# Kernel tuning notes

Measured on AMD Instinct MI355X. Metric: run time of the kernel, lower is better.

The kernel has to match this reference:

```python
import jax, jax.numpy as jnp
import numpy as np

H = W = 128  # render resolution (init height/width)
EPS = 1e-8

def _normalize(x, axis):
    return x / (jnp.linalg.norm(x, axis=axis, keepdims=True) + EPS)

def _render_one(pts, camrot, campos, proj, uv, faces):
    # pts (p,3), camrot (3,3), campos (3,), proj (3,1), uv (p,2), faces (f,3)
    pc = (pts - campos) @ camrot.T                       # camera-space verts (p,3)
    xy = pc[:, :2] * proj[:2, 0] / (pc[:, 2:3] + EPS)    # perspective projection -> NDC (p,2)
    v3d = pc[faces]                                      # (f,3,3)
    v2d = xy[faces]                                      # (f,3,2)
    n = jnp.cross(v3d[:, 1] - v3d[:, 0], v3d[:, 2] - v3d[:, 0])  # face normals (f,3)
    n1 = _normalize(n, axis=1)
    # pixel grid in NDC
    px = jnp.linspace(-1.0, 1.0, W)[None, None, :]
    py = jnp.linspace(1.0, -1.0, H)[None, :, None]
    ax, ay = v2d[:, 0, 0, None, None], v2d[:, 0, 1, None, None]
    bx, by = v2d[:, 1, 0, None, None], v2d[:, 1, 1, None, None]
    cx, cy = v2d[:, 2, 0, None, None], v2d[:, 2, 1, None, None]
    d = (by - cy) * (ax - cx) + (cx - bx) * (ay - cy)    # (f,1,1) signed 2*area
    l0 = ((by - cy) * (px - cx) + (cx - bx) * (py - cy)) / (d + EPS)
    l1 = ((cy - ay) * (px - cx) + (ax - cx) * (py - cy)) / (d + EPS)
    l2 = 1.0 - l0 - l1                                   # barycentrics (f,H,W)
    z = (l0 * v3d[:, 0, 2, None, None] + l1 * v3d[:, 1, 2, None, None]
         + l2 * v3d[:, 2, 2, None, None])                # interpolated depth (f,H,W)
    inside = (l0 >= 0) & (l1 >= 0) & (l2 >= 0) & (jnp.abs(d) > EPS) & (z > EPS)
    zm = jnp.where(inside, z, jnp.float32(1e10))
    idx = jnp.argmin(zm, axis=0)                         # nearest visible face per pixel (H,W)
    hard = jnp.any(inside, axis=0)[..., None].astype(pts.dtype)  # hardmask (H,W,1)
    take = lambda a: jnp.take_along_axis(a, idx[None], axis=0)[0]  # (H,W)
    uvsel = uv[faces][idx]                               # (H,W,3,2) per-pixel face uvs
    tc = (take(l0)[..., None] * uvsel[..., 0, :]
          + take(l1)[..., None] * uvsel[..., 1, :]
          + take(l2)[..., None] * uvsel[..., 2, :]) * hard  # imtexcoords (H,W,2)
    return tc, hard, n1

def _fragment_shader(tc, texture, mask):
    # nearest-filter texture lookup; texture (3,th,tw)
    th, tw = texture.shape[1], texture.shape[2]
    u = jnp.clip(tc[..., 0], 0.0, 1.0)
    v = jnp.clip(tc[..., 1], 0.0, 1.0)
    tx = jnp.round(u * (tw - 1)).astype(jnp.int32)
    ty = jnp.round((1.0 - v) * (th - 1)).astype(jnp.int32)
    color = texture[:, ty, tx].transpose(1, 2, 0)        # (H,W,3)
    return color * mask

def setup_inputs() -> dict:
    key = jax.random.key(0)
    ks = jax.random.split(key, 6)
    b, p, f = 3, 768, 1024
    points = jax.random.normal(ks[0], (b, p, 3), jnp.float32) * 0.3
    faces = jax.random.randint(ks[1], (f, 3), 0, p)
    camera_rot = jnp.broadcast_to(jnp.eye(3, dtype=jnp.float32), (b, 3, 3))
    camera_pos = jnp.zeros((b, 3), jnp.float32).at[:, 2].set(-3.0)  # objects in front of camera
    camera_proj = jnp.ones((3, 1), jnp.float32)
    uv = jax.random.uniform(ks[2], (b, p, 2), jnp.float32)
    texture = jax.random.uniform(ks[3], (b, 3, 512, 512), jnp.float32)
    ts = jax.random.normal(ks[4], (b, 3), jnp.float32)
    return dict(points=points, camera_rot=camera_rot, camera_pos=camera_pos,
                camera_proj=camera_proj, uv=uv, texture=texture, ts=ts, faces=faces)

def reference(points, camera_rot, camera_pos, camera_proj, uv, texture, ts, faces):
    b = points.shape[0]
    render = jax.vmap(_render_one, in_axes=(0, 0, 0, None, 0, None))
    tcs, masks, normals = render(points, camera_rot, camera_pos, camera_proj, uv, faces)
    ims = jax.vmap(_fragment_shader)(tcs, texture, masks)   # (b,H,W,3)
    probs = masks                                            # improb proxy == hardmask
    order = jnp.argsort(-ts[:, 2])                           # far -> near compositing order
    ims_s, probs_s, masks_s = ims[order], probs[order], masks[order]
    imrender, improb, fg = ims_s[0], probs_s[0], masks_s[0]
    for i in range(1, b):                                    # fixed small layer count
        m = masks_s[i] > 0.5
        imrender = jnp.where(m, ims_s[i], imrender)
        improb = jnp.where(m, probs_s[i], improb)
        fg = jnp.where(m, masks_s[i], fg)
    return imrender[None], improb[None], normals, fg[None]
```

## Files before the change

### kernel.cpp

```cpp
#include <hip/hip_runtime.h>
#include <math.h>

#define B_ 3
#define P_ 768
#define F_ 1024
#define H_ 128
#define W_ 128
#define HW_ (H_*W_)
#define EPS_ 1e-8f

#define OFF_PROB   49152
#define OFF_NORM   65536
#define OFF_FG     74752


__global__ __launch_bounds__(256) void raster_fwd(
    const float* __restrict__ points,
    const float* __restrict__ camrot,
    const float* __restrict__ campos,
    const float* __restrict__ proj,
    const int*   __restrict__ faces,
    float4* __restrict__ faceE,
    const float* __restrict__ uv,
    unsigned long long* __restrict__ packed,
    float*  __restrict__ normals_out)
{
#pragma clang fp contract(off)
    int wid  = blockIdx.x * 4 + (threadIdx.x >> 6);
    int sub  = blockIdx.y;
    int lane = threadIdx.x & 63;
    int b = wid / F_;
    int f = wid - b * F_;

    const float* R = camrot + b * 9;
    float cpx = campos[b*3+0], cpy = campos[b*3+1], cpz = campos[b*3+2];
    float pj0 = proj[0], pj1 = proj[1];

    int idx3[3];
    float pcx[3], pcy[3], pcz[3], sx[3], sy[3];
    for (int v = 0; v < 3; ++v) {
        int vi = faces[f*3 + v];
        idx3[v] = vi;
        const float* P = points + (b*P_ + vi) * 3;
        float vx = P[0] - cpx;
        float vy = P[1] - cpy;
        float vz = P[2] - cpz;
        float qx = (vx*R[0] + vy*R[1]) + vz*R[2];
        float qy = (vx*R[3] + vy*R[4]) + vz*R[5];
        float qz = (vx*R[6] + vy*R[7]) + vz*R[8];
        pcx[v] = qx; pcy[v] = qy; pcz[v] = qz;
        float dz = qz + EPS_;
        sx[v] = (qx * pj0) / dz;
        sy[v] = (qy * pj1) / dz;
    }

    float ax = sx[0], ay = sy[0];
    float bx = sx[1], by = sy[1];
    float cx = sx[2], cy = sy[2];

    float e0x = by - cy;
    float e0y = cx - bx;
    float e1x = cy - ay;
    float e1y = ax - cx;
    float d = e0x*(ax - cx) + e0y*(ay - cy);
    float denom = d + EPS_;
    bool valid = fabsf(d) > EPS_;
    float z0 = pcz[0], z1 = pcz[1], z2 = pcz[2];

    if (lane == 0 && sub == 0) {
        float4* rec = faceE + wid * 4;
        rec[0] = make_float4(e0x, e0y, e1x, e1y);
        rec[1] = make_float4(cx, cy, denom, valid ? 1.0f : 0.0f);
        const float* uvb = uv + b * P_ * 2;
        rec[2] = make_float4(uvb[idx3[0]*2+0], uvb[idx3[0]*2+1],
                             uvb[idx3[1]*2+0], uvb[idx3[1]*2+1]);
        rec[3] = make_float4(uvb[idx3[2]*2+0], uvb[idx3[2]*2+1], 0.0f, 0.0f);

        float ux = pcx[1]-pcx[0], uy = pcy[1]-pcy[0], uz = pcz[1]-pcz[0];
        float wx = pcx[2]-pcx[0], wy = pcy[2]-pcy[0], wz = pcz[2]-pcz[0];
        float nx = fmaf(uy, wz, -(uz*wy));
        float ny = fmaf(uz, wx, -(ux*wz));
        float nz = fmaf(ux, wy, -(uy*wx));
        float nn = sqrtf((nx*nx + ny*ny) + nz*nz) + 1e-8f;
        normals_out[wid*3+0] = nx / nn;
        normals_out[wid*3+1] = ny / nn;
        normals_out[wid*3+2] = nz / nn;
    }

    if (!valid) return;

    float gx0 = (ax + 1.0f) * 63.5f;
    float gx1 = (bx + 1.0f) * 63.5f;
    float gx2 = (cx + 1.0f) * 63.5f;
    float gy0 = (1.0f - ay) * 63.5f;
    float gy1 = (1.0f - by) * 63.5f;
    float gy2 = (1.0f - cy) * 63.5f;
    int xlo = max(0,   (int)ceilf (fminf(fminf(gx0,gx1),gx2) - 1.0f));
    int xhi = min(127, (int)floorf(fmaxf(fmaxf(gx0,gx1),gx2) + 1.0f));
    int ylo = max(0,   (int)ceilf (fminf(fminf(gy0,gy1),gy2) - 1.0f));
    int yhi = min(127, (int)floorf(fmaxf(fmaxf(gy0,gy1),gy2) + 1.0f));
    int wX = xhi - xlo + 1;
    int wY = yhi - ylo + 1;
    if (wX <= 0 || wY <= 0) return;
    int N = wX * wY;

    int i0 = sub * 64 + lane;
    if (i0 >= N) return;
    int q = 128 / wX;
    int r = 128 - q * wX;
    int yy = i0 / wX;
    int xx = i0 - yy * wX;

    const double STEP = 2.0 / 127.0;
    unsigned long long* cells = packed + b * HW_;

    for (int i = i0; i < N; i += 128) {
        int X = xlo + xx;
        int Y = ylo + yy;
        float px = (float)(-1.0 + (double)X * STEP);
        float py = (float)( 1.0 - (double)Y * STEP);
        float dx = px - cx;
        float dy = py - cy;
        float n0 = e0x*dx + e0y*dy;
        float n1 = e1x*dx + e1y*dy;
        float l0 = n0 / denom;
        float l1 = n1 / denom;
        float l2 = 1.0f - l0 - l1;
        float zz = (l0*z0 + l1*z1) + l2*z2;
        if (l0 >= 0.0f && l1 >= 0.0f && l2 >= 0.0f && zz > EPS_) {
            unsigned long long pk =
                ((unsigned long long)__float_as_uint(zz) << 32) | (unsigned)f;
            atomicMin(&cells[Y * W_ + X], pk);
        }
        xx += r; yy += q;
        if (xx >= wX) { xx -= wX; yy += 1; }
    }
}

__global__ __launch_bounds__(64) void shade_composite(
    const float4* __restrict__ faceE,
    const float*  __restrict__ tex,
    const float*  __restrict__ ts,
    const unsigned long long* __restrict__ packed,
    float* __restrict__ out)
{
#pragma clang fp contract(off)
    int pix = blockIdx.x * 64 + threadIdx.x;
    int y = pix >> 7;
    int x = pix & (W_ - 1);

    const double STEP = 2.0 / 127.0;
    float px = (float)(-1.0 + (double)x * STEP);
    float py = (float)( 1.0 - (double)y * STEP);

    const unsigned MISS_BITS = __float_as_uint(1e10f);

    unsigned long long pka = packed[0 * HW_ + pix];
    unsigned long long pkb = packed[1 * HW_ + pix];
    unsigned long long pkc = packed[2 * HW_ + pix];

    float k0 = ts[0*3+2], k1 = ts[1*3+2], k2 = ts[2*3+2];
    int o0 = 0, o1 = 1, o2 = 2;
    if (k1 > k0) { int ti=o0; o0=o1; o1=ti; float tf=k0; k0=k1; k1=tf; }
    if (k2 > k1) { int ti=o1; o1=o2; o2=ti; float tf=k1; k1=k2; k2=tf; }
    if (k1 > k0) { int ti=o0; o0=o1; o1=ti; float tf=k0; k0=k1; k1=tf; }

    unsigned long long p0 = (o0 == 0) ? pka : ((o0 == 1) ? pkb : pkc);
    unsigned long long p1 = (o1 == 0) ? pka : ((o1 == 1) ? pkb : pkc);
    unsigned long long p2 = (o2 == 0) ? pka : ((o2 == 1) ? pkb : pkc);
    bool h1 = (unsigned)(p1 >> 32) < MISS_BITS;
    bool h2 = (unsigned)(p2 >> 32) < MISS_BITS;

    int w = o0; unsigned long long pkw = p0;
    if (h1) { w = o1; pkw = p1; }
    if (h2) { w = o2; pkw = p2; }
    bool hardw = (unsigned)(pkw >> 32) < MISS_BITS;

    float sr = 0.0f, sg = 0.0f, sb = 0.0f, sm = 0.0f;
    if (hardw) {
        int fi = (int)(unsigned)pkw;
        const float4* rec = faceE + (w * F_ + fi) * 4;
        float4 A  = rec[0];
        float4 Bv = rec[1];
        float4 Cv = rec[2];
        float4 Dv = rec[3];

        float dx = px - Bv.x;
        float dy = py - Bv.y;
        float n0 = A.x*dx + A.y*dy;
        float n1 = A.z*dx + A.w*dy;
        float l0 = n0 / Bv.z;
        float l1 = n1 / Bv.z;
        float l2 = 1.0f - l0 - l1;
        float tu = (l0*Cv.x + l1*Cv.z) + l2*Dv.x;
        float tv = (l0*Cv.y + l1*Cv.w) + l2*Dv.y;
        float uc = fminf(fmaxf(tu, 0.0f), 1.0f);
        float vc = fminf(fmaxf(tv, 0.0f), 1.0f);
        int txi = (int)rintf(uc * 511.0f);
        int tyi = (int)rintf((1.0f - vc) * 511.0f);

        const float* tb = tex + w * 3 * 262144;
        int o = tyi*512 + txi;
        sr = tb[0*262144 + o];
        sg = tb[1*262144 + o];
        sb = tb[2*262144 + o];
        sm = 1.0f;
    }

    out[pix*3+0] = sr;
    out[pix*3+1] = sg;
    out[pix*3+2] = sb;
    out[OFF_PROB + pix] = sm;
    out[OFF_FG   + pix] = sm;
}

extern "C" void kernel_launch(void* const* d_in, const int* in_sizes, int n_in,
                              void* d_out, int out_size, void* d_ws, size_t ws_size,
                              hipStream_t stream) {
    const float* points = (const float*)d_in[0];
    const float* camrot = (const float*)d_in[1];
    const float* campos = (const float*)d_in[2];
    const float* proj   = (const float*)d_in[3];
    const float* uv     = (const float*)d_in[4];
    const float* tex    = (const float*)d_in[5];
    const float* ts     = (const float*)d_in[6];
    const int*   faces  = (const int*)d_in[7];
    float* out = (float*)d_out;

    char* ws = (char*)d_ws;
    float4* faceE = (float4*)(ws);
    unsigned long long* packed = (unsigned long long*)(ws + 196608);


    raster_fwd<<<dim3(B_*F_/4, 2), dim3(256), 0, stream>>>(
        points, camrot, campos, proj, faces, faceE, uv,
        packed, out + OFF_NORM);
    shade_composite<<<dim3(HW_/64), dim3(64), 0, stream>>>(
        faceE, tex, ts, packed, out);
}
```

Baseline: 83.83 us.

## Set up faces once per block and rasterize 16 faces with whole-block pixel loops

Raster work is remapped so each 256-thread block handles 16 faces. The first 16 threads compute the projection, edge equations, bounding box, face record and normal once per face and stage them in shared memory. After a block barrier, all 256 threads sweep each face's bounding box in turn. This removes the redundant per-lane setup (previously every lane of 2x64 threads recomputed each face) and the split grid. In exchange the grid shrinks to 192 blocks, faces inside a block are processed one after another, and small faces leave most threads idle.

```diff
diff --git a/kernel.cpp b/kernel.cpp
--- a/kernel.cpp
+++ b/kernel.cpp
@@ -8,6 +8,7 @@
 #define W_ 128
 #define HW_ (H_*W_)
 #define EPS_ 1e-8f
+#define FPB_ 16
 
 #define OFF_PROB   49152
 #define OFF_NORM   65536
@@ -26,48 +27,52 @@
     float*  __restrict__ normals_out)
 {
 #pragma clang fp contract(off)
-    int wid  = blockIdx.x * 4 + (threadIdx.x >> 6);
-    int sub  = blockIdx.y;
-    int lane = threadIdx.x & 63;
-    int b = wid / F_;
-    int f = wid - b * F_;
-
-    const float* R = camrot + b * 9;
-    float cpx = campos[b*3+0], cpy = campos[b*3+1], cpz = campos[b*3+2];
-    float pj0 = proj[0], pj1 = proj[1];
-
-    int idx3[3];
-    float pcx[3], pcy[3], pcz[3], sx[3], sy[3];
-    for (int v = 0; v < 3; ++v) {
-        int vi = faces[f*3 + v];
-        idx3[v] = vi;
-        const float* P = points + (b*P_ + vi) * 3;
-        float vx = P[0] - cpx;
-        float vy = P[1] - cpy;
-        float vz = P[2] - cpz;
-        float qx = (vx*R[0] + vy*R[1]) + vz*R[2];
-        float qy = (vx*R[3] + vy*R[4]) + vz*R[5];
-        float qz = (vx*R[6] + vy*R[7]) + vz*R[8];
-        pcx[v] = qx; pcy[v] = qy; pcz[v] = qz;
-        float dz = qz + EPS_;
-        sx[v] = (qx * pj0) / dz;
-        sy[v] = (qy * pj1) / dz;
-    }
-
-    float ax = sx[0], ay = sy[0];
-    float bx = sx[1], by = sy[1];
-    float cx = sx[2], cy = sy[2];
-
-    float e0x = by - cy;
-    float e0y = cx - bx;
-    float e1x = cy - ay;
-    float e1y = ax - cx;
-    float d = e0x*(ax - cx) + e0y*(ay - cy);
-    float denom = d + EPS_;
-    bool valid = fabsf(d) > EPS_;
-    float z0 = pcz[0], z1 = pcz[1], z2 = pcz[2];
-
-    if (lane == 0 && sub == 0) {
+    int tid = threadIdx.x;
+    int b   = blockIdx.x >> 6;
+
+    __shared__ float sE0x[FPB_], sE0y[FPB_], sE1x[FPB_], sE1y[FPB_];
+    __shared__ float sCx[FPB_],  sCy[FPB_],  sDen[FPB_];
+    __shared__ float sZ0[FPB_],  sZ1[FPB_],  sZ2[FPB_];
+    __shared__ int   sXlo[FPB_], sYlo[FPB_], sWX[FPB_], sN[FPB_];
+
+    if (tid < FPB_) {
+        int wid = blockIdx.x * FPB_ + tid;
+        int f   = wid - b * F_;
+
+        const float* R = camrot + b * 9;
+        float cpx = campos[b*3+0], cpy = campos[b*3+1], cpz = campos[b*3+2];
+        float pj0 = proj[0], pj1 = proj[1];
+
+        int idx3[3];
+        float pcx[3], pcy[3], pcz[3], sx[3], sy[3];
+        for (int v = 0; v < 3; ++v) {
+            int vi = faces[f*3 + v];
+            idx3[v] = vi;
+            const float* P = points + (b*P_ + vi) * 3;
+            float vx = P[0] - cpx;
+            float vy = P[1] - cpy;
+            float vz = P[2] - cpz;
+            float qx = (vx*R[0] + vy*R[1]) + vz*R[2];
+            float qy = (vx*R[3] + vy*R[4]) + vz*R[5];
+            float qz = (vx*R[6] + vy*R[7]) + vz*R[8];
+            pcx[v] = qx; pcy[v] = qy; pcz[v] = qz;
+            float dz = qz + EPS_;
+            sx[v] = (qx * pj0) / dz;
+            sy[v] = (qy * pj1) / dz;
+        }
+
+        float ax = sx[0], ay = sy[0];
+        float bx = sx[1], by = sy[1];
+        float cx = sx[2], cy = sy[2];
+
+        float e0x = by - cy;
+        float e0y = cx - bx;
+        float e1x = cy - ay;
+        float e1y = ax - cx;
+        float d = e0x*(ax - cx) + e0y*(ay - cy);
+        float denom = d + EPS_;
+        bool valid = fabsf(d) > EPS_;
+
         float4* rec = faceE + wid * 4;
         rec[0] = make_float4(e0x, e0y, e1x, e1y);
         rec[1] = make_float4(cx, cy, denom, valid ? 1.0f : 0.0f);
@@ -85,55 +90,71 @@
         normals_out[wid*3+0] = nx / nn;
         normals_out[wid*3+1] = ny / nn;
         normals_out[wid*3+2] = nz / nn;
+
+        int N = 0, xlo = 0, ylo = 0, wX = 1;
+        if (valid) {
+            float gx0 = (ax + 1.0f) * 63.5f;
+            float gx1 = (bx + 1.0f) * 63.5f;
+            float gx2 = (cx + 1.0f) * 63.5f;
+            float gy0 = (1.0f - ay) * 63.5f;
+            float gy1 = (1.0f - by) * 63.5f;
+            float gy2 = (1.0f - cy) * 63.5f;
+            xlo = max(0,   (int)ceilf (fminf(fminf(gx0,gx1),gx2) - 1.0f));
+            int xhi = min(127, (int)floorf(fmaxf(fmaxf(gx0,gx1),gx2) + 1.0f));
+            ylo = max(0,   (int)ceilf (fminf(fminf(gy0,gy1),gy2) - 1.0f));
+            int yhi = min(127, (int)floorf(fmaxf(fmaxf(gy0,gy1),gy2) + 1.0f));
+            int wXl = xhi - xlo + 1;
+            int wYl = yhi - ylo + 1;
+            if (wXl > 0 && wYl > 0) { N = wXl * wYl; wX = wXl; }
+        }
+        sE0x[tid] = e0x; sE0y[tid] = e0y; sE1x[tid] = e1x; sE1y[tid] = e1y;
+        sCx[tid]  = cx;  sCy[tid]  = cy;  sDen[tid] = denom;
+        sZ0[tid]  = pcz[0]; sZ1[tid] = pcz[1]; sZ2[tid] = pcz[2];
+        sXlo[tid] = xlo; sYlo[tid] = ylo; sWX[tid] = wX; sN[tid] = N;
     }
-
-    if (!valid) return;
-
-    float gx0 = (ax + 1.0f) * 63.5f;
-    float gx1 = (bx + 1.0f) * 63.5f;
-    float gx2 = (cx + 1.0f) * 63.5f;
-    float gy0 = (1.0f - ay) * 63.5f;
-    float gy1 = (1.0f - by) * 63.5f;
-    float gy2 = (1.0f - cy) * 63.5f;
-    int xlo = max(0,   (int)ceilf (fminf(fminf(gx0,gx1),gx2) - 1.0f));
-    int xhi = min(127, (int)floorf(fmaxf(fmaxf(gx0,gx1),gx2) + 1.0f));
-    int ylo = max(0,   (int)ceilf (fminf(fminf(gy0,gy1),gy2) - 1.0f));
-    int yhi = min(127, (int)floorf(fmaxf(fmaxf(gy0,gy1),gy2) + 1.0f));
-    int wX = xhi - xlo + 1;
-    int wY = yhi - ylo + 1;
-    if (wX <= 0 || wY <= 0) return;
-    int N = wX * wY;
-
-    int i0 = sub * 64 + lane;
-    if (i0 >= N) return;
-    int q = 128 / wX;
-    int r = 128 - q * wX;
-    int yy = i0 / wX;
-    int xx = i0 - yy * wX;
+    __syncthreads();
 
     const double STEP = 2.0 / 127.0;
     unsigned long long* cells = packed + b * HW_;
-
-    for (int i = i0; i < N; i += 128) {
-        int X = xlo + xx;
-        int Y = ylo + yy;
-        float px = (float)(-1.0 + (double)X * STEP);
-        float py = (float)( 1.0 - (double)Y * STEP);
-        float dx = px - cx;
-        float dy = py - cy;
-        float n0 = e0x*dx + e0y*dy;
-        float n1 = e1x*dx + e1y*dy;
-        float l0 = n0 / denom;
-        float l1 = n1 / denom;
-        float l2 = 1.0f - l0 - l1;
-        float zz = (l0*z0 + l1*z1) + l2*z2;
-        if (l0 >= 0.0f && l1 >= 0.0f && l2 >= 0.0f && zz > EPS_) {
-            unsigned long long pk =
-                ((unsigned long long)__float_as_uint(zz) << 32) | (unsigned)f;
-            atomicMin(&cells[Y * W_ + X], pk);
+    int fbase = (blockIdx.x & 63) * FPB_;
+
+    for (int fl = 0; fl < FPB_; ++fl) {
+        int N = sN[fl];
+        if (tid >= N) continue;
+
+        float e0x = sE0x[fl], e0y = sE0y[fl], e1x = sE1x[fl], e1y = sE1y[fl];
+        float cx  = sCx[fl],  cy  = sCy[fl],  denom = sDen[fl];
+        float z0  = sZ0[fl],  z1  = sZ1[fl],  z2 = sZ2[fl];
+        int xlo = sXlo[fl], ylo = sYlo[fl];
+        unsigned f = (unsigned)(fbase + fl);
+
+        unsigned uwX = (unsigned)sWX[fl];
+        unsigned q = 256u / uwX;
+        unsigned r = 256u - q * uwX;
+        unsigned yy = (unsigned)tid / uwX;
+        unsigned xx = (unsigned)tid - yy * uwX;
+
+        for (int i = tid; i < N; i += 256) {
+            int X = xlo + (int)xx;
+            int Y = ylo + (int)yy;
+            float px = (float)(-1.0 + (double)X * STEP);
+            float py = (float)( 1.0 - (double)Y * STEP);
+            float dx = px - cx;
+            float dy = py - cy;
+            float n0 = e0x*dx + e0y*dy;
+            float n1 = e1x*dx + e1y*dy;
+            float l0 = n0 / denom;
+            float l1 = n1 / denom;
+            float l2 = 1.0f - l0 - l1;
+            float zz = (l0*z0 + l1*z1) + l2*z2;
+            if (l0 >= 0.0f && l1 >= 0.0f && l2 >= 0.0f && zz > EPS_) {
+                unsigned long long pk =
+                    ((unsigned long long)__float_as_uint(zz) << 32) | f;
+                atomicMin(&cells[Y * W_ + X], pk);
+            }
+            xx += r; yy += q;
+            if (xx >= uwX) { xx -= uwX; yy += 1; }
         }
-        xx += r; yy += q;
-        if (xx >= wX) { xx -= wX; yy += 1; }
     }
 }
 
@@ -232,7 +253,7 @@
     unsigned long long* packed = (unsigned long long*)(ws + 196608);
 
 
-    raster_fwd<<<dim3(B_*F_/4, 2), dim3(256), 0, stream>>>(
+    raster_fwd<<<dim3(B_*F_/FPB_), dim3(256), 0, stream>>>(
         points, camrot, campos, proj, faces, faceE, uv,
         packed, out + OFF_NORM);
     shade_composite<<<dim3(HW_/64), dim3(64), 0, stream>>>(
```

Measured after the change: 82.98 us (median of 2 runs). About the same (-1.0%).
